# Optimization experiments

Measured on AMD Instinct MI355X. Metric: run time of the kernel, lower is better.

Reference implementation:

```python
import jax, jax.numpy as jnp
import numpy as np

N = 50000
E = 800000
IN = 3
H = 64
OUT = 128
L = 4


def _layernorm(x, w, b, eps=1e-5):
    mu = jnp.mean(x, axis=-1, keepdims=True)
    var = jnp.mean(jnp.square(x - mu), axis=-1, keepdims=True)
    return (x - mu) * jax.lax.rsqrt(var + eps) * w + b


def setup_inputs() -> dict:
    key = jax.random.key(0)
    ks = jax.random.split(key, 12)

    def lin(k, fan_in, shape):
        return jax.random.normal(k, shape, dtype=jnp.float32) / np.sqrt(fan_in)

    x = jax.random.normal(ks[0], (N, IN), dtype=jnp.float32)
    edge_index = jax.random.randint(ks[1], (2, E), 0, N, dtype=jnp.int32)
    return {
        "x": x,
        "edge_index": edge_index,
        "in_w": lin(ks[2], IN, (IN, H)), "in_b": jnp.zeros((H,), jnp.float32),
        "ew1": lin(ks[3], 2, (2, H)), "eb1": jnp.zeros((H,), jnp.float32),
        "ew2": lin(ks[4], H, (H, H)), "eb2": jnp.zeros((H,), jnp.float32),
        "cw1": lin(ks[5], H, (L, H, H)), "cb1": jnp.zeros((L, H), jnp.float32),
        "cw2": lin(ks[6], H, (L, H, H)), "cb2": jnp.zeros((L, H), jnp.float32),
        "lnw": jnp.ones((L, H), jnp.float32), "lnb": jnp.zeros((L, H), jnp.float32),
        "fw": lin(ks[7], H, (H, OUT)), "fb": jnp.zeros((OUT,), jnp.float32),
        "rw": lin(ks[8], H, (H, OUT)), "rb": jnp.zeros((OUT,), jnp.float32),
        "ow": jnp.ones((OUT,), jnp.float32), "ob": jnp.zeros((OUT,), jnp.float32),
    }


def reference(x, edge_index, in_w, in_b, ew1, eb1, ew2, eb2,
              cw1, cb1, cw2, cb2, lnw, lnb, fw, fb, rw, rb, ow, ob):
    pos = x[:, :2]
    row, col = edge_index[0], edge_index[1]  # source, target (PyG convention)
    rel_pos = pos[col] - pos[row]                              # [E, 2]
    edge_attr = jnp.maximum(rel_pos @ ew1 + eb1, 0.0) @ ew2 + eb2  # [E, H]

    h = x @ in_w + in_b  # [N, H]
    for i in range(L):
        identity = h
        # GINEConv (eps=0): mlp(x_i + sum_j relu(x_j + e_ij))
        msg = jax.nn.relu(h[row] + edge_attr)                  # [E, H]
        agg = jax.ops.segment_sum(msg, col, num_segments=N)    # [N, H]
        m = h + agg
        m = jnp.maximum(m @ cw1[i] + cb1[i], 0.0) @ cw2[i] + cb2[i]
        m = _layernorm(m, lnw[i], lnb[i])
        h = jax.nn.gelu(m, approximate=False) + identity

    out = (h @ fw + fb) + (h @ rw + rb)
    return _layernorm(out, ow, ob)
```

## Files before the change

### kernel.cpp

```cpp
#include <hip/hip_runtime.h>
#include <hip/hip_fp16.h>
#include <stdint.h>

#define NN 50000
#define NE 800000
#define SCAN_BLOCKS 196

typedef _Float16 half8v __attribute__((ext_vector_type(8)));
typedef float f32x4 __attribute__((ext_vector_type(4)));

static __device__ __forceinline__ __half2 u2h2(unsigned int u) {
    union { unsigned int u; __half2 h; } c; c.u = u; return c.h;
}
static __device__ __forceinline__ unsigned int h22u(__half2 h) {
    union { __half2 h; unsigned int u; } c; c.h = h; return c.u;
}

static __device__ __forceinline__ float4 fma4(float4 a, float s, float4 w) {
    a.x = fmaf(s, w.x, a.x); a.y = fmaf(s, w.y, a.y);
    a.z = fmaf(s, w.z, a.z); a.w = fmaf(s, w.w, a.w);
    return a;
}
static __device__ __forceinline__ void acc8(float* acc, float4 hv, float4 ev) {
    const unsigned int* hu = (const unsigned int*)&hv;
    const unsigned int* eu = (const unsigned int*)&ev;
    #pragma unroll
    for (int q = 0; q < 4; ++q) {
        float2 hf = __half22float2(u2h2(hu[q]));
        float2 ef = __half22float2(u2h2(eu[q]));
        acc[q * 2]     += fmaxf(hf.x + ef.x, 0.f);
        acc[q * 2 + 1] += fmaxf(hf.y + ef.y, 0.f);
    }
}

__global__ __launch_bounds__(256) void k_deg(const int* __restrict__ ei, int* __restrict__ offcur) {
    int e = blockIdx.x * 256 + threadIdx.x;
    atomicAdd(&offcur[ei[NE + e]], 1);
}

__global__ __launch_bounds__(256) void k_scanA(const int* __restrict__ off, int* __restrict__ part) {
    __shared__ int s[256];
    int t = threadIdx.x;
    int idx = blockIdx.x * 256 + t;
    int d = (idx < NN) ? off[idx] : 0;
    s[t] = d; __syncthreads();
    for (int o = 128; o > 0; o >>= 1) {
        if (t < o) s[t] += s[t + o];
        __syncthreads();
    }
    if (t == 0) part[blockIdx.x] = s[0];
}

__global__ __launch_bounds__(256) void k_scanB(int* __restrict__ part) {
    __shared__ int s[256];
    int t = threadIdx.x;
    int d = (t < SCAN_BLOCKS) ? part[t] : 0;
    s[t] = d; __syncthreads();
    #pragma unroll
    for (int o = 1; o < 256; o <<= 1) {
        int v = (t >= o) ? s[t - o] : 0;
        __syncthreads();
        s[t] += v;
        __syncthreads();
    }
    if (t < SCAN_BLOCKS) part[t] = s[t] - d;
}

__global__ __launch_bounds__(256) void k_scanC(int* __restrict__ off, const int* __restrict__ part) {
    __shared__ int s[256];
    int t = threadIdx.x;
    int idx = blockIdx.x * 256 + t;
    int d = (idx < NN) ? off[idx] : 0;
    s[t] = d; __syncthreads();
    #pragma unroll
    for (int o = 1; o < 256; o <<= 1) {
        int v = (t >= o) ? s[t - o] : 0;
        __syncthreads();
        s[t] += v;
        __syncthreads();
    }
    if (idx < NN) off[idx] = s[t] - d + part[blockIdx.x];
}

__global__ __launch_bounds__(256) void k_prep(const float* __restrict__ ew2, __half* __restrict__ w2f) {
    int tid = threadIdx.x;
    for (int i = tid; i < 4096; i += 256) {
        int k = i >> 6, n = i & 63;
        int kt = k >> 5, kin = k & 31;
        int quad = kin >> 3, j = kin & 7;
        int nt = n >> 4, nin = n & 15;
        w2f[(size_t)((kt * 4 + nt) * 64 + quad * 16 + nin) * 8 + j] = __float2half(ew2[i]);
    }
}

__global__ __launch_bounds__(256) void k_input(const float* __restrict__ x,
        const float* __restrict__ in_w, const float* __restrict__ in_b,
        __half* __restrict__ Ah) {
    int n = blockIdx.x * 4 + (threadIdx.x >> 6);
    int k = threadIdx.x & 63;
    const float* xr = x + (size_t)n * 3;
    float v = in_b[k] + xr[0] * in_w[k] + xr[1] * in_w[64 + k] + xr[2] * in_w[128 + k];
    Ah[(size_t)n * 64 + k] = __float2half(v);
}

__global__ __launch_bounds__(256) void k_edge(const float* __restrict__ x,
        const int* __restrict__ ei,
        const float* __restrict__ ew1, const float* __restrict__ eb1,
        const float* __restrict__ eb2, const __half* __restrict__ w2f,
        int* __restrict__ offcur, unsigned short* __restrict__ rows,
        __half* __restrict__ ea) {
    __shared__ float s_w1[128], s_b1[64], s_b2[64];
    __shared__ float s_rx[256], s_ry[256];
    __shared__ int s_pos[256];
    __shared__ __half s_d[4][16][80];
    int tid = threadIdx.x, lane = tid & 63, w = tid >> 6;

    half8v bf[8];
    {
        const half8v* W2F = (const half8v*)w2f;
        #pragma unroll
        for (int f = 0; f < 8; ++f) bf[f] = W2F[f * 64 + lane];
    }
    if (tid < 128) s_w1[tid] = ew1[tid];
    if (tid < 64) s_b1[tid] = eb1[tid];
    else if (tid < 128) s_b2[tid - 64] = eb2[tid - 64];
    int eb = blockIdx.x * 256;
    {
        int e = eb + tid;
        int r = ei[e], c = ei[NE + e];
        s_rx[tid] = x[(size_t)c * 3]     - x[(size_t)r * 3];
        s_ry[tid] = x[(size_t)c * 3 + 1] - x[(size_t)r * 3 + 1];
        int pos = atomicAdd(&offcur[c], 1);
        rows[pos] = (unsigned short)r;
        s_pos[tid] = pos;
    }
    __syncthreads();

    int lm = lane & 15, lq = lane >> 4;
    #pragma unroll
    for (int t = 0; t < 4; ++t) {
        int ebase = w * 64 + t * 16;
        float rx = s_rx[ebase + lm], ry = s_ry[ebase + lm];
        half8v a0, a1;
        #pragma unroll
        for (int j = 0; j < 8; ++j) {
            int k0 = lq * 8 + j;
            a0[j] = (_Float16)fmaxf(fmaf(rx, s_w1[k0], fmaf(ry, s_w1[64 + k0], s_b1[k0])), 0.f);
            int k1 = k0 + 32;
            a1[j] = (_Float16)fmaxf(fmaf(rx, s_w1[k1], fmaf(ry, s_w1[64 + k1], s_b1[k1])), 0.f);
        }
        f32x4 acc[4];
        #pragma unroll
        for (int nt = 0; nt < 4; ++nt) {
            float b = s_b2[nt * 16 + lm];
            acc[nt][0] = b; acc[nt][1] = b; acc[nt][2] = b; acc[nt][3] = b;
            acc[nt] = __builtin_amdgcn_mfma_f32_16x16x32_f16(a0, bf[nt],     acc[nt], 0, 0, 0);
            acc[nt] = __builtin_amdgcn_mfma_f32_16x16x32_f16(a1, bf[4 + nt], acc[nt], 0, 0, 0);
        }
        __builtin_amdgcn_wave_barrier();
        #pragma unroll
        for (int nt = 0; nt < 4; ++nt)
            #pragma unroll
            for (int r = 0; r < 4; ++r)
                s_d[w][lq * 4 + r][nt * 16 + lm] = __float2half(acc[nt][r]);
        __builtin_amdgcn_wave_barrier();
        int row = lane >> 2, seg = lane & 3;
        int pos = s_pos[w * 64 + t * 16 + row];
        uint4 v0 = *(const uint4*)&s_d[w][row][seg * 16];
        uint4 v1 = *(const uint4*)&s_d[w][row][seg * 16 + 8];
        uint4* dst = (uint4*)&ea[(size_t)pos * 64 + seg * 16];
        dst[0] = v0;
        dst[1] = v1;
        __builtin_amdgcn_wave_barrier();
    }
}

__global__ __launch_bounds__(256) void k_agg(const __half* __restrict__ Ah,
        const __half* __restrict__ ea, const unsigned short* __restrict__ rows,
        const int* __restrict__ offcur, __half* __restrict__ M) {
    const float4* A4 = (const float4*)Ah;
    const float4* E4 = (const float4*)ea;
    int w = threadIdx.x >> 6, lane = threadIdx.x & 63;
    int es = lane >> 3, oc = lane & 7;
    int n = blockIdx.x * 4 + w;
    int p0 = (n == 0) ? 0 : offcur[n - 1];
    int p1 = offcur[n];
    float acc[8] = {0,0,0,0,0,0,0,0};
    float accB[8] = {0,0,0,0,0,0,0,0};
    for (int base = p0; base < p1; base += 64) {
        int cnt = min(64, p1 - base);
        int rl = (int)rows[base + min(lane, cnt - 1)];
        int j = 0;
        for (; j + 16 <= cnt; j += 16) {
            int i0 = j + es, i1 = j + 8 + es;
            int r0 = __shfl(rl, i0, 64);
            int r1 = __shfl(rl, i1, 64);
            float4 h0 = A4[(size_t)r0 * 8 + oc];
            float4 h1 = A4[(size_t)r1 * 8 + oc];
            float4 e0 = E4[(size_t)(base + i0) * 8 + oc];
            float4 e1 = E4[(size_t)(base + i1) * 8 + oc];
            acc8(acc, h0, e0);
            acc8(accB, h1, e1);
        }
        for (; j < cnt; j += 8) {
            int i0 = j + es;
            bool valid = i0 < cnt;
            int ic = valid ? i0 : (cnt - 1);
            int r0 = __shfl(rl, ic, 64);
            float4 h0 = A4[(size_t)r0 * 8 + oc];
            float4 e0 = E4[(size_t)(base + ic) * 8 + oc];
            if (valid) acc8(acc, h0, e0);
        }
    }
    #pragma unroll
    for (int q = 0; q < 8; ++q) acc[q] += accB[q];
    #pragma unroll
    for (int m = 8; m < 64; m <<= 1) {
        #pragma unroll
        for (int q = 0; q < 8; ++q) acc[q] += __shfl_xor(acc[q], m, 64);
    }
    if (es == 0) {
        float4 sv = A4[(size_t)n * 8 + oc];
        const unsigned int* su = (const unsigned int*)&sv;
        unsigned int o[4];
        #pragma unroll
        for (int q = 0; q < 4; ++q) {
            float2 sf = __half22float2(u2h2(su[q]));
            o[q] = h22u(__floats2half2_rn(sf.x + acc[q * 2], sf.y + acc[q * 2 + 1]));
        }
        *(uint4*)&M[(size_t)n * 64 + oc * 8] = *(uint4*)&o[0];
    }
}

__global__ __launch_bounds__(256) void k_node(__half* __restrict__ Ah, const __half* __restrict__ M,
        const float* __restrict__ cw1, const float* __restrict__ cb1,
        const float* __restrict__ cw2, const float* __restrict__ cb2,
        const float* __restrict__ lnw, const float* __restrict__ lnb) {
    __shared__ float s_W1[64 * 64];
    __shared__ float s_W2[64 * 64];
    __shared__ float s_m[64 * 68];
    __shared__ float s_b1[64], s_b2[64], s_g[64], s_bt[64];
    int tid = threadIdx.x;
    for (int i = tid; i < 4096; i += 256) { s_W1[i] = cw1[i]; s_W2[i] = cw2[i]; }
    if (tid < 64) { s_b1[tid] = cb1[tid]; s_g[tid] = lnw[tid]; }
    else if (tid < 128) { s_b2[tid - 64] = cb2[tid - 64]; s_bt[tid - 64] = lnb[tid - 64]; }
    int nb = blockIdx.x * 64;
    {
        const uint4* M4 = (const uint4*)(M + (size_t)nb * 64);
        #pragma unroll
        for (int q = 0; q < 2; ++q) {
            int i = q * 256 + tid;
            int nl = i >> 3;
            int k8 = (i & 7) * 8;
            uint4 v = {0, 0, 0, 0};
            if (nb + nl < NN) v = M4[i];
            float* dst = &s_m[nl * 68 + k8];
            const unsigned int* vu = (const unsigned int*)&v;
            #pragma unroll
            for (int p = 0; p < 4; ++p) {
                float2 f = __half22float2(u2h2(vu[p]));
                dst[p * 2] = f.x; dst[p * 2 + 1] = f.y;
            }
        }
    }
    __syncthreads();

    int lane = tid & 63, w = tid >> 6;
    int cq = lane & 15, ng = lane >> 4;
    int rbase = w * 16 + ng * 4;
    int c0 = cq * 4;

    float4 acc[4];
    {
        float4 b1q = *(const float4*)&s_b1[c0];
        acc[0] = b1q; acc[1] = b1q; acc[2] = b1q; acc[3] = b1q;
    }
    #pragma unroll 4
    for (int k4 = 0; k4 < 16; ++k4) {
        float4 m0 = *(const float4*)&s_m[(rbase + 0) * 68 + k4 * 4];
        float4 m1 = *(const float4*)&s_m[(rbase + 1) * 68 + k4 * 4];
        float4 m2 = *(const float4*)&s_m[(rbase + 2) * 68 + k4 * 4];
        float4 m3 = *(const float4*)&s_m[(rbase + 3) * 68 + k4 * 4];
        #pragma unroll
        for (int kk = 0; kk < 4; ++kk) {
            float4 w4 = *(const float4*)&s_W1[(k4 * 4 + kk) * 64 + c0];
            acc[0] = fma4(acc[0], ((const float*)&m0)[kk], w4);
            acc[1] = fma4(acc[1], ((const float*)&m1)[kk], w4);
            acc[2] = fma4(acc[2], ((const float*)&m2)[kk], w4);
            acc[3] = fma4(acc[3], ((const float*)&m3)[kk], w4);
        }
    }
    __builtin_amdgcn_wave_barrier();
    #pragma unroll
    for (int j = 0; j < 4; ++j) {
        float4 u;
        u.x = fmaxf(acc[j].x, 0.f); u.y = fmaxf(acc[j].y, 0.f);
        u.z = fmaxf(acc[j].z, 0.f); u.w = fmaxf(acc[j].w, 0.f);
        *(float4*)&s_m[(rbase + j) * 68 + c0] = u;
    }
    __builtin_amdgcn_wave_barrier();

    {
        float4 b2q = *(const float4*)&s_b2[c0];
        acc[0] = b2q; acc[1] = b2q; acc[2] = b2q; acc[3] = b2q;
    }
    #pragma unroll 4
    for (int k4 = 0; k4 < 16; ++k4) {
        float4 m0 = *(const float4*)&s_m[(rbase + 0) * 68 + k4 * 4];
        float4 m1 = *(const float4*)&s_m[(rbase + 1) * 68 + k4 * 4];
        float4 m2 = *(const float4*)&s_m[(rbase + 2) * 68 + k4 * 4];
        float4 m3 = *(const float4*)&s_m[(rbase + 3) * 68 + k4 * 4];
        #pragma unroll
        for (int kk = 0; kk < 4; ++kk) {
            float4 w4 = *(const float4*)&s_W2[(k4 * 4 + kk) * 64 + c0];
            acc[0] = fma4(acc[0], ((const float*)&m0)[kk], w4);
            acc[1] = fma4(acc[1], ((const float*)&m1)[kk], w4);
            acc[2] = fma4(acc[2], ((const float*)&m2)[kk], w4);
            acc[3] = fma4(acc[3], ((const float*)&m3)[kk], w4);
        }
    }

    float4 gq  = *(const float4*)&s_g[c0];
    float4 btq = *(const float4*)&s_bt[c0];
    #pragma unroll
    for (int j = 0; j < 4; ++j) {
        float4 v = acc[j];
        float sum = v.x + v.y + v.z + v.w;
        float sq  = v.x * v.x + v.y * v.y + v.z * v.z + v.w * v.w;
        #pragma unroll
        for (int m = 1; m < 16; m <<= 1) {
            sum += __shfl_xor(sum, m, 64);
            sq  += __shfl_xor(sq, m, 64);
        }
        float mu  = sum * (1.f / 64.f);
        float var = sq * (1.f / 64.f) - mu * mu;
        float rs  = rsqrtf(var + 1e-5f);
        int n = nb + rbase + j;
        if (n < NN) {
            uint2 iu = *(const uint2*)&Ah[(size_t)n * 64 + c0];
            float2 i0 = __half22float2(u2h2(iu.x));
            float2 i1 = __half22float2(u2h2(iu.y));
            float4 o;
            float y;
            y = (v.x - mu) * rs * gq.x + btq.x; o.x = 0.5f * y * (1.f + erff(y * 0.70710678118654752f)) + i0.x;
            y = (v.y - mu) * rs * gq.y + btq.y; o.y = 0.5f * y * (1.f + erff(y * 0.70710678118654752f)) + i0.y;
            y = (v.z - mu) * rs * gq.z + btq.z; o.z = 0.5f * y * (1.f + erff(y * 0.70710678118654752f)) + i1.x;
            y = (v.w - mu) * rs * gq.w + btq.w; o.w = 0.5f * y * (1.f + erff(y * 0.70710678118654752f)) + i1.y;
            uint2 ou;
            ou.x = h22u(__floats2half2_rn(o.x, o.y));
            ou.y = h22u(__floats2half2_rn(o.z, o.w));
            *(uint2*)&Ah[(size_t)n * 64 + c0] = ou;
        }
    }
}

__global__ __launch_bounds__(256) void k_final(const __half* __restrict__ Ah,
        const float* __restrict__ fw, const float* __restrict__ fb,
        const float* __restrict__ rw, const float* __restrict__ rb,
        const float* __restrict__ ow, const float* __restrict__ ob,
        float* __restrict__ out) {
    __shared__ float s_W[64 * 128];
    __shared__ float s_h[32 * 68];
    __shared__ float s_b[128];
    __shared__ float s_red[32][4];
    int tid = threadIdx.x;
    for (int i = tid; i < 8192; i += 256) s_W[i] = fw[i] + rw[i];
    if (tid < 128) s_b[tid] = fb[tid] + rb[tid];
    int nb = blockIdx.x * 32;
    for (int i = tid; i < 2048; i += 256) {
        int nl = i >> 6, k = i & 63;
        int n = nb + nl;
        s_h[nl * 68 + k] = (n < NN) ? __half2float(Ah[(size_t)n * 64 + k]) : 0.f;
    }
    __syncthreads();

    int lane = tid & 63, w = tid >> 6;
    int chh = w & 1, nh = w >> 1;
    int cq = lane & 15, ng = lane >> 4;
    int c0 = chh * 64 + cq * 4;
    int rbase = nh * 16 + ng * 4;

    float4 acc[4];
    {
        float4 bq = *(const float4*)&s_b[c0];
        acc[0] = bq; acc[1] = bq; acc[2] = bq; acc[3] = bq;
    }
    #pragma unroll 4
    for (int k4 = 0; k4 < 16; ++k4) {
        float4 m0 = *(const float4*)&s_h[(rbase + 0) * 68 + k4 * 4];
        float4 m1 = *(const float4*)&s_h[(rbase + 1) * 68 + k4 * 4];
        float4 m2 = *(const float4*)&s_h[(rbase + 2) * 68 + k4 * 4];
        float4 m3 = *(const float4*)&s_h[(rbase + 3) * 68 + k4 * 4];
        #pragma unroll
        for (int kk = 0; kk < 4; ++kk) {
            float4 w4 = *(const float4*)&s_W[(k4 * 4 + kk) * 128 + c0];
            acc[0] = fma4(acc[0], ((const float*)&m0)[kk], w4);
            acc[1] = fma4(acc[1], ((const float*)&m1)[kk], w4);
            acc[2] = fma4(acc[2], ((const float*)&m2)[kk], w4);
            acc[3] = fma4(acc[3], ((const float*)&m3)[kk], w4);
        }
    }
    #pragma unroll
    for (int j = 0; j < 4; ++j) {
        float4 v = acc[j];
        float sum = v.x + v.y + v.z + v.w;
        float sq  = v.x * v.x + v.y * v.y + v.z * v.z + v.w * v.w;
        #pragma unroll
        for (int m = 1; m < 16; m <<= 1) {
            sum += __shfl_xor(sum, m, 64);
            sq  += __shfl_xor(sq, m, 64);
        }
        if (cq == 0) {
            s_red[rbase + j][chh * 2]     = sum;
            s_red[rbase + j][chh * 2 + 1] = sq;
        }
    }
    __syncthreads();
    float4 gq = *(const float4*)&ow[c0];
    float4 bq = *(const float4*)&ob[c0];
    #pragma unroll
    for (int j = 0; j < 4; ++j) {
        int nl = rbase + j;
        int n = nb + nl;
        float tsum = s_red[nl][0] + s_red[nl][2];
        float tsq  = s_red[nl][1] + s_red[nl][3];
        float mu  = tsum * (1.f / 128.f);
        float var = tsq * (1.f / 128.f) - mu * mu;
        float rs  = rsqrtf(var + 1e-5f);
        if (n < NN) {
            float4 v = acc[j];
            float4 o;
            o.x = (v.x - mu) * rs * gq.x + bq.x;
            o.y = (v.y - mu) * rs * gq.y + bq.y;
            o.z = (v.z - mu) * rs * gq.z + bq.z;
            o.w = (v.w - mu) * rs * gq.w + bq.w;
            *(float4*)&out[(size_t)n * 128 + c0] = o;
        }
    }
}

extern "C" void kernel_launch(void* const* d_in, const int* in_sizes, int n_in,
                              void* d_out, int out_size, void* d_ws, size_t ws_size,
                              hipStream_t stream) {
    const float* x    = (const float*)d_in[0];
    const int*   ei   = (const int*)d_in[1];
    const float* in_w = (const float*)d_in[2];
    const float* in_b = (const float*)d_in[3];
    const float* ew1  = (const float*)d_in[4];
    const float* eb1  = (const float*)d_in[5];
    const float* ew2  = (const float*)d_in[6];
    const float* eb2  = (const float*)d_in[7];
    const float* cw1  = (const float*)d_in[8];
    const float* cb1  = (const float*)d_in[9];
    const float* cw2  = (const float*)d_in[10];
    const float* cb2  = (const float*)d_in[11];
    const float* lnw  = (const float*)d_in[12];
    const float* lnb  = (const float*)d_in[13];
    const float* fw   = (const float*)d_in[14];
    const float* fb   = (const float*)d_in[15];
    const float* rw   = (const float*)d_in[16];
    const float* rb   = (const float*)d_in[17];
    const float* ow   = (const float*)d_in[18];
    const float* ob   = (const float*)d_in[19];
    float* out = (float*)d_out;

    char* ws = (char*)d_ws;
    __half*         ea   = (__half*)ws;
    __half*         Ah   = (__half*)(ws + 102400000);
    unsigned short* rows = (unsigned short*)(ws + 108800000);
    int*            off  = (int*)(ws + 110400000);
    __half*         M    = (__half*)(ws + 110600016);
    int*            part = (int*)M;
    __half*         w2f  = (__half*)((char*)M + 100000);

    (void)hipMemsetAsync(off, 0, (NN + 1) * sizeof(int), stream);
    k_deg<<<NE / 256, 256, 0, stream>>>(ei, off);
    k_scanA<<<SCAN_BLOCKS, 256, 0, stream>>>(off, part);
    k_scanB<<<1, 256, 0, stream>>>(part);
    k_scanC<<<SCAN_BLOCKS, 256, 0, stream>>>(off, part);
    k_prep<<<1, 256, 0, stream>>>(ew2, w2f);
    k_input<<<NN / 4, 256, 0, stream>>>(x, in_w, in_b, Ah);
    k_edge<<<NE / 256, 256, 0, stream>>>(x, ei, ew1, eb1, eb2, w2f, off, rows, ea);

    const int nodeBlocks = (NN + 63) / 64;
    for (int l = 0; l < 4; ++l) {
        k_agg<<<NN / 4, 256, 0, stream>>>(Ah, ea, rows, off, M);
        k_node<<<nodeBlocks, 256, 0, stream>>>(Ah, M,
            cw1 + (size_t)l * 4096, cb1 + (size_t)l * 64,
            cw2 + (size_t)l * 4096, cb2 + (size_t)l * 64,
            lnw + (size_t)l * 64,   lnb + (size_t)l * 64);
    }
    k_final<<<(NN + 31) / 32, 256, 0, stream>>>(Ah, fw, fb, rw, rb, ow, ob, out);
}
```

Measured before the change: 477.4 us.

## Fuse edge aggregation into node MLP kernel with ping-pong feature buffers

Merges the per-layer aggregation kernel into the node MLP/LayerNorm kernel. Each block gathers neighbour messages for its 64 nodes directly into shared memory in fp32, which removes the intermediate fp16 M buffer round trip and one launch per layer. Two feature buffers are now ping-ponged so no block overwrites features that other blocks still read. The rows store in the edge kernel is also moved after the MFMA work. The trade-off is fewer blocks (782 instead of 12500) and less parallelism for the irregular gather. The weight staging also now shares a block with the latency-bound gather.

Result: slower. 614.9 us (+28.8%).

```diff
diff --git a/kernel.cpp b/kernel.cpp
--- a/kernel.cpp
+++ b/kernel.cpp
@@ -125,13 +125,14 @@
     if (tid < 64) s_b1[tid] = eb1[tid];
     else if (tid < 128) s_b2[tid - 64] = eb2[tid - 64];
     int eb = blockIdx.x * 256;
+    int my_r, my_pos;
     {
         int e = eb + tid;
         int r = ei[e], c = ei[NE + e];
         s_rx[tid] = x[(size_t)c * 3]     - x[(size_t)r * 3];
         s_ry[tid] = x[(size_t)c * 3 + 1] - x[(size_t)r * 3 + 1];
         int pos = atomicAdd(&offcur[c], 1);
-        rows[pos] = (unsigned short)r;
+        my_r = r; my_pos = pos;
         s_pos[tid] = pos;
     }
     __syncthreads();
@@ -173,66 +174,13 @@
         dst[1] = v1;
         __builtin_amdgcn_wave_barrier();
     }
-}
-
-__global__ __launch_bounds__(256) void k_agg(const __half* __restrict__ Ah,
+    rows[my_pos] = (unsigned short)my_r;
+}
+
+__global__ __launch_bounds__(256) void k_layer(const __half* __restrict__ Ain,
+        __half* __restrict__ Aout,
         const __half* __restrict__ ea, const unsigned short* __restrict__ rows,
-        const int* __restrict__ offcur, __half* __restrict__ M) {
-    const float4* A4 = (const float4*)Ah;
-    const float4* E4 = (const float4*)ea;
-    int w = threadIdx.x >> 6, lane = threadIdx.x & 63;
-    int es = lane >> 3, oc = lane & 7;
-    int n = blockIdx.x * 4 + w;
-    int p0 = (n == 0) ? 0 : offcur[n - 1];
-    int p1 = offcur[n];
-    float acc[8] = {0,0,0,0,0,0,0,0};
-    float accB[8] = {0,0,0,0,0,0,0,0};
-    for (int base = p0; base < p1; base += 64) {
-        int cnt = min(64, p1 - base);
-        int rl = (int)rows[base + min(lane, cnt - 1)];
-        int j = 0;
-        for (; j + 16 <= cnt; j += 16) {
-            int i0 = j + es, i1 = j + 8 + es;
-            int r0 = __shfl(rl, i0, 64);
-            int r1 = __shfl(rl, i1, 64);
-            float4 h0 = A4[(size_t)r0 * 8 + oc];
-            float4 h1 = A4[(size_t)r1 * 8 + oc];
-            float4 e0 = E4[(size_t)(base + i0) * 8 + oc];
-            float4 e1 = E4[(size_t)(base + i1) * 8 + oc];
-            acc8(acc, h0, e0);
-            acc8(accB, h1, e1);
-        }
-        for (; j < cnt; j += 8) {
-            int i0 = j + es;
-            bool valid = i0 < cnt;
-            int ic = valid ? i0 : (cnt - 1);
-            int r0 = __shfl(rl, ic, 64);
-            float4 h0 = A4[(size_t)r0 * 8 + oc];
-            float4 e0 = E4[(size_t)(base + ic) * 8 + oc];
-            if (valid) acc8(acc, h0, e0);
-        }
-    }
-    #pragma unroll
-    for (int q = 0; q < 8; ++q) acc[q] += accB[q];
-    #pragma unroll
-    for (int m = 8; m < 64; m <<= 1) {
-        #pragma unroll
-        for (int q = 0; q < 8; ++q) acc[q] += __shfl_xor(acc[q], m, 64);
-    }
-    if (es == 0) {
-        float4 sv = A4[(size_t)n * 8 + oc];
-        const unsigned int* su = (const unsigned int*)&sv;
-        unsigned int o[4];
-        #pragma unroll
-        for (int q = 0; q < 4; ++q) {
-            float2 sf = __half22float2(u2h2(su[q]));
-            o[q] = h22u(__floats2half2_rn(sf.x + acc[q * 2], sf.y + acc[q * 2 + 1]));
-        }
-        *(uint4*)&M[(size_t)n * 64 + oc * 8] = *(uint4*)&o[0];
-    }
-}
-
-__global__ __launch_bounds__(256) void k_node(__half* __restrict__ Ah, const __half* __restrict__ M,
+        const int* __restrict__ off,
         const float* __restrict__ cw1, const float* __restrict__ cb1,
         const float* __restrict__ cw2, const float* __restrict__ cb2,
         const float* __restrict__ lnw, const float* __restrict__ lnb) {
@@ -244,28 +192,72 @@
     for (int i = tid; i < 4096; i += 256) { s_W1[i] = cw1[i]; s_W2[i] = cw2[i]; }
     if (tid < 64) { s_b1[tid] = cb1[tid]; s_g[tid] = lnw[tid]; }
     else if (tid < 128) { s_b2[tid - 64] = cb2[tid - 64]; s_bt[tid - 64] = lnb[tid - 64]; }
+
     int nb = blockIdx.x * 64;
-    {
-        const uint4* M4 = (const uint4*)(M + (size_t)nb * 64);
-        #pragma unroll
-        for (int q = 0; q < 2; ++q) {
-            int i = q * 256 + tid;
-            int nl = i >> 3;
-            int k8 = (i & 7) * 8;
-            uint4 v = {0, 0, 0, 0};
-            if (nb + nl < NN) v = M4[i];
-            float* dst = &s_m[nl * 68 + k8];
-            const unsigned int* vu = (const unsigned int*)&v;
+    int lane = tid & 63, w = tid >> 6;
+
+    {
+        const float4* A4 = (const float4*)Ain;
+        const float4* E4 = (const float4*)ea;
+        int es = lane >> 3, oc = lane & 7;
+        for (int t = 0; t < 16; ++t) {
+            int nl = w * 16 + t;
+            int n = nb + nl;
+            float acc[8] = {0,0,0,0,0,0,0,0};
+            float accB[8] = {0,0,0,0,0,0,0,0};
+            int p0 = 0, p1 = 0;
+            if (n < NN) { p0 = (n == 0) ? 0 : off[n - 1]; p1 = off[n]; }
+            for (int base = p0; base < p1; base += 64) {
+                int cnt = min(64, p1 - base);
+                int rl = (int)rows[base + min(lane, cnt - 1)];
+                int j = 0;
+                for (; j + 16 <= cnt; j += 16) {
+                    int i0 = j + es, i1 = j + 8 + es;
+                    int r0 = __shfl(rl, i0, 64);
+                    int r1 = __shfl(rl, i1, 64);
+                    float4 h0 = A4[(size_t)r0 * 8 + oc];
+                    float4 h1 = A4[(size_t)r1 * 8 + oc];
+                    float4 e0 = E4[(size_t)(base + i0) * 8 + oc];
+                    float4 e1 = E4[(size_t)(base + i1) * 8 + oc];
+                    acc8(acc, h0, e0);
+                    acc8(accB, h1, e1);
+                }
+                for (; j < cnt; j += 8) {
+                    int i0 = j + es;
+                    bool valid = i0 < cnt;
+                    int ic = valid ? i0 : (cnt - 1);
+                    int r0 = __shfl(rl, ic, 64);
+                    float4 h0 = A4[(size_t)r0 * 8 + oc];
+                    float4 e0 = E4[(size_t)(base + ic) * 8 + oc];
+                    if (valid) acc8(acc, h0, e0);
+                }
+            }
             #pragma unroll
-            for (int p = 0; p < 4; ++p) {
-                float2 f = __half22float2(u2h2(vu[p]));
-                dst[p * 2] = f.x; dst[p * 2 + 1] = f.y;
+            for (int q = 0; q < 8; ++q) acc[q] += accB[q];
+            #pragma unroll
+            for (int m = 8; m < 64; m <<= 1) {
+                #pragma unroll
+                for (int q = 0; q < 8; ++q) acc[q] += __shfl_xor(acc[q], m, 64);
             }
+            if (es == 0) {
+                if (n < NN) {
+                    float4 sv = A4[(size_t)n * 8 + oc];
+                    const unsigned int* su = (const unsigned int*)&sv;
+                    #pragma unroll
+                    for (int q = 0; q < 4; ++q) {
+                        float2 sf = __half22float2(u2h2(su[q]));
+                        acc[q * 2]     += sf.x;
+                        acc[q * 2 + 1] += sf.y;
+                    }
+                }
+                float* dst = &s_m[nl * 68 + oc * 8];
+                *(float4*)dst       = *(float4*)&acc[0];
+                *(float4*)(dst + 4) = *(float4*)&acc[4];
+            }
         }
     }
     __syncthreads();
 
-    int lane = tid & 63, w = tid >> 6;
     int cq = lane & 15, ng = lane >> 4;
     int rbase = w * 16 + ng * 4;
     int c0 = cq * 4;
@@ -337,7 +329,7 @@
         float rs  = rsqrtf(var + 1e-5f);
         int n = nb + rbase + j;
         if (n < NN) {
-            uint2 iu = *(const uint2*)&Ah[(size_t)n * 64 + c0];
+            uint2 iu = *(const uint2*)&Ain[(size_t)n * 64 + c0];
             float2 i0 = __half22float2(u2h2(iu.x));
             float2 i1 = __half22float2(u2h2(iu.y));
             float4 o;
@@ -349,7 +341,7 @@
             uint2 ou;
             ou.x = h22u(__floats2half2_rn(o.x, o.y));
             ou.y = h22u(__floats2half2_rn(o.z, o.w));
-            *(uint2*)&Ah[(size_t)n * 64 + c0] = ou;
+            *(uint2*)&Aout[(size_t)n * 64 + c0] = ou;
         }
     }
 }
@@ -466,12 +458,12 @@
 
     char* ws = (char*)d_ws;
     __half*         ea   = (__half*)ws;
-    __half*         Ah   = (__half*)(ws + 102400000);
-    unsigned short* rows = (unsigned short*)(ws + 108800000);
-    int*            off  = (int*)(ws + 110400000);
-    __half*         M    = (__half*)(ws + 110600016);
-    int*            part = (int*)M;
-    __half*         w2f  = (__half*)((char*)M + 100000);
+    __half*         Ah0  = (__half*)(ws + 102400000);
+    __half*         Ah1  = (__half*)(ws + 108800000);
+    unsigned short* rows = (unsigned short*)(ws + 115200000);
+    int*            off  = (int*)(ws + 116800000);
+    int*            part = (int*)(ws + 117000016);
+    __half*         w2f  = (__half*)(ws + 117100016);
 
     (void)hipMemsetAsync(off, 0, (NN + 1) * sizeof(int), stream);
     k_deg<<<NE / 256, 256, 0, stream>>>(ei, off);
@@ -479,16 +471,18 @@
     k_scanB<<<1, 256, 0, stream>>>(part);
     k_scanC<<<SCAN_BLOCKS, 256, 0, stream>>>(off, part);
     k_prep<<<1, 256, 0, stream>>>(ew2, w2f);
-    k_input<<<NN / 4, 256, 0, stream>>>(x, in_w, in_b, Ah);
+    k_input<<<NN / 4, 256, 0, stream>>>(x, in_w, in_b, Ah0);
     k_edge<<<NE / 256, 256, 0, stream>>>(x, ei, ew1, eb1, eb2, w2f, off, rows, ea);
 
     const int nodeBlocks = (NN + 63) / 64;
+    __half* Ain = Ah0;
+    __half* Aout = Ah1;
     for (int l = 0; l < 4; ++l) {
-        k_agg<<<NN / 4, 256, 0, stream>>>(Ah, ea, rows, off, M);
-        k_node<<<nodeBlocks, 256, 0, stream>>>(Ah, M,
+        k_layer<<<nodeBlocks, 256, 0, stream>>>(Ain, Aout, ea, rows, off,
             cw1 + (size_t)l * 4096, cb1 + (size_t)l * 64,
             cw2 + (size_t)l * 4096, cb2 + (size_t)l * 64,
             lnw + (size_t)l * 64,   lnb + (size_t)l * 64);
-    }
-    k_final<<<(NN + 31) / 32, 256, 0, stream>>>(Ah, fw, fb, rw, rb, ow, ob, out);
-}
+        __half* tmp = Ain; Ain = Aout; Aout = tmp;
+    }
+    k_final<<<(NN + 31) / 32, 256, 0, stream>>>(Ain, fw, fb, rw, rb, ow, ob, out);
+}
```

## Use fp16 MFMA for node MLP with prepacked conv weights

Applied to the files above, without the earlier changes.

The node-update kernel now runs both 64x64 matmuls on MFMA 16x16x32 f16 instructions instead of fp32 FMA loops. It reads weights that k_prep (now 9 blocks) converts once into fp16 fragment layout, and LayerNorm statistics are reduced from the MFMA accumulator layout. This removes the per-block fp32 weight staging into LDS (32KB) and the scalar FMA work, at the cost of fp16 rounding of the hidden activation. Separately, the rows[] scatter store in k_edge is moved to the end of the kernel.

After: 406.4 us. 14.9% less time.

```diff
diff --git a/kernel.cpp b/kernel.cpp
--- a/kernel.cpp
+++ b/kernel.cpp
@@ -82,14 +82,24 @@
     if (idx < NN) off[idx] = s[t] - d + part[blockIdx.x];
 }
 
-__global__ __launch_bounds__(256) void k_prep(const float* __restrict__ ew2, __half* __restrict__ w2f) {
+__global__ __launch_bounds__(256) void k_prep(const float* __restrict__ ew2,
+        const float* __restrict__ cw1, const float* __restrict__ cw2,
+        __half* __restrict__ wf) {
+    int b = blockIdx.x;
+    const float* src;
+    if (b == 0) src = ew2;
+    else {
+        int l = (b - 1) >> 1;
+        src = ((b - 1) & 1) ? (cw2 + (size_t)l * 4096) : (cw1 + (size_t)l * 4096);
+    }
+    __half* dst = wf + (size_t)b * 4096;
     int tid = threadIdx.x;
     for (int i = tid; i < 4096; i += 256) {
         int k = i >> 6, n = i & 63;
         int kt = k >> 5, kin = k & 31;
         int quad = kin >> 3, j = kin & 7;
         int nt = n >> 4, nin = n & 15;
-        w2f[(size_t)((kt * 4 + nt) * 64 + quad * 16 + nin) * 8 + j] = __float2half(ew2[i]);
+        dst[(size_t)((kt * 4 + nt) * 64 + quad * 16 + nin) * 8 + j] = __float2half(src[i]);
     }
 }
 
@@ -125,13 +135,14 @@
     if (tid < 64) s_b1[tid] = eb1[tid];
     else if (tid < 128) s_b2[tid - 64] = eb2[tid - 64];
     int eb = blockIdx.x * 256;
+    int my_r, my_pos;
     {
         int e = eb + tid;
         int r = ei[e], c = ei[NE + e];
         s_rx[tid] = x[(size_t)c * 3]     - x[(size_t)r * 3];
         s_ry[tid] = x[(size_t)c * 3 + 1] - x[(size_t)r * 3 + 1];
         int pos = atomicAdd(&offcur[c], 1);
-        rows[pos] = (unsigned short)r;
+        my_r = r; my_pos = pos;
         s_pos[tid] = pos;
     }
     __syncthreads();
@@ -173,6 +184,7 @@
         dst[1] = v1;
         __builtin_amdgcn_wave_barrier();
     }
+    rows[my_pos] = (unsigned short)my_r;
 }
 
 __global__ __launch_bounds__(256) void k_agg(const __half* __restrict__ Ah,
@@ -233,123 +245,109 @@
 }
 
 __global__ __launch_bounds__(256) void k_node(__half* __restrict__ Ah, const __half* __restrict__ M,
-        const float* __restrict__ cw1, const float* __restrict__ cb1,
-        const float* __restrict__ cw2, const float* __restrict__ cb2,
+        const __half* __restrict__ w1f, const __half* __restrict__ w2f,
+        const float* __restrict__ cb1, const float* __restrict__ cb2,
         const float* __restrict__ lnw, const float* __restrict__ lnb) {
-    __shared__ float s_W1[64 * 64];
-    __shared__ float s_W2[64 * 64];
-    __shared__ float s_m[64 * 68];
+    __shared__ __half s_u[4][16][72];
     __shared__ float s_b1[64], s_b2[64], s_g[64], s_bt[64];
-    int tid = threadIdx.x;
-    for (int i = tid; i < 4096; i += 256) { s_W1[i] = cw1[i]; s_W2[i] = cw2[i]; }
+    int tid = threadIdx.x, lane = tid & 63, w = tid >> 6;
+    int lm = lane & 15, lq = lane >> 4;
+
+    half8v bw1[8], bw2[8];
+    {
+        const half8v* W1F = (const half8v*)w1f;
+        const half8v* W2F = (const half8v*)w2f;
+        #pragma unroll
+        for (int f = 0; f < 8; ++f) { bw1[f] = W1F[f * 64 + lane]; bw2[f] = W2F[f * 64 + lane]; }
+    }
     if (tid < 64) { s_b1[tid] = cb1[tid]; s_g[tid] = lnw[tid]; }
     else if (tid < 128) { s_b2[tid - 64] = cb2[tid - 64]; s_bt[tid - 64] = lnb[tid - 64]; }
+    __syncthreads();
+
     int nb = blockIdx.x * 64;
-    {
-        const uint4* M4 = (const uint4*)(M + (size_t)nb * 64);
-        #pragma unroll
-        for (int q = 0; q < 2; ++q) {
-            int i = q * 256 + tid;
-            int nl = i >> 3;
-            int k8 = (i & 7) * 8;
-            uint4 v = {0, 0, 0, 0};
-            if (nb + nl < NN) v = M4[i];
-            float* dst = &s_m[nl * 68 + k8];
-            const unsigned int* vu = (const unsigned int*)&v;
+    int na = nb + w * 16 + lm;
+    int nac = min(na, NN - 1);
+
+    const uint4* M4 = (const uint4*)M;
+    uint4 a0u = M4[(size_t)nac * 8 + lq];
+    uint4 a1u = M4[(size_t)nac * 8 + 4 + lq];
+    half8v a0 = *(const half8v*)&a0u;
+    half8v a1 = *(const half8v*)&a1u;
+
+    f32x4 acc[4];
+    #pragma unroll
+    for (int nt = 0; nt < 4; ++nt) {
+        float b = s_b1[nt * 16 + lm];
+        acc[nt][0] = b; acc[nt][1] = b; acc[nt][2] = b; acc[nt][3] = b;
+        acc[nt] = __builtin_amdgcn_mfma_f32_16x16x32_f16(a0, bw1[nt],     acc[nt], 0, 0, 0);
+        acc[nt] = __builtin_amdgcn_mfma_f32_16x16x32_f16(a1, bw1[4 + nt], acc[nt], 0, 0, 0);
+    }
+    __builtin_amdgcn_wave_barrier();
+    #pragma unroll
+    for (int nt = 0; nt < 4; ++nt)
+        #pragma unroll
+        for (int r = 0; r < 4; ++r)
+            s_u[w][lq * 4 + r][nt * 16 + lm] = __float2half(fmaxf(acc[nt][r], 0.f));
+    __builtin_amdgcn_wave_barrier();
+
+    half8v u0 = *(const half8v*)&s_u[w][lm][lq * 8];
+    half8v u1 = *(const half8v*)&s_u[w][lm][32 + lq * 8];
+    #pragma unroll
+    for (int nt = 0; nt < 4; ++nt) {
+        float b = s_b2[nt * 16 + lm];
+        acc[nt][0] = b; acc[nt][1] = b; acc[nt][2] = b; acc[nt][3] = b;
+        acc[nt] = __builtin_amdgcn_mfma_f32_16x16x32_f16(u0, bw2[nt],     acc[nt], 0, 0, 0);
+        acc[nt] = __builtin_amdgcn_mfma_f32_16x16x32_f16(u1, bw2[4 + nt], acc[nt], 0, 0, 0);
+    }
+
+    float S[4], SQ[4];
+    #pragma unroll
+    for (int r = 0; r < 4; ++r) {
+        S[r]  = acc[0][r] + acc[1][r] + acc[2][r] + acc[3][r];
+        SQ[r] = acc[0][r] * acc[0][r] + acc[1][r] * acc[1][r]
+              + acc[2][r] * acc[2][r] + acc[3][r] * acc[3][r];
+    }
+    #pragma unroll
+    for (int m = 1; m < 16; m <<= 1) {
+        #pragma unroll
+        for (int r = 0; r < 4; ++r) {
+            S[r]  += __shfl_xor(S[r], m, 64);
+            SQ[r] += __shfl_xor(SQ[r], m, 64);
+        }
+    }
+    __builtin_amdgcn_wave_barrier();
+    #pragma unroll
+    for (int r = 0; r < 4; ++r) {
+        float mu  = S[r] * (1.f / 64.f);
+        float var = SQ[r] * (1.f / 64.f) - mu * mu;
+        float rs  = rsqrtf(var + 1e-5f);
+        #pragma unroll
+        for (int nt = 0; nt < 4; ++nt) {
+            int c = nt * 16 + lm;
+            float y = (acc[nt][r] - mu) * rs * s_g[c] + s_bt[c];
+            float ge = 0.5f * y * (1.f + erff(y * 0.70710678118654752f));
+            s_u[w][lq * 4 + r][c] = __float2half(ge);
+        }
+    }
+    __builtin_amdgcn_wave_barrier();
+
+    #pragma unroll
+    for (int it = 0; it < 2; ++it) {
+        int ck = lq + 4 * it;
+        int n = nb + w * 16 + lm;
+        if (n < NN) {
+            uint4 ge8 = *(const uint4*)&s_u[w][lm][ck * 8];
+            uint4 id8 = *(const uint4*)&Ah[(size_t)n * 64 + ck * 8];
+            const unsigned int* gu = (const unsigned int*)&ge8;
+            const unsigned int* iu = (const unsigned int*)&id8;
+            unsigned int o[4];
             #pragma unroll
             for (int p = 0; p < 4; ++p) {
-                float2 f = __half22float2(u2h2(vu[p]));
-                dst[p * 2] = f.x; dst[p * 2 + 1] = f.y;
+                float2 gf = __half22float2(u2h2(gu[p]));
+                float2 iff = __half22float2(u2h2(iu[p]));
+                o[p] = h22u(__floats2half2_rn(gf.x + iff.x, gf.y + iff.y));
             }
-        }
-    }
-    __syncthreads();
-
-    int lane = tid & 63, w = tid >> 6;
-    int cq = lane & 15, ng = lane >> 4;
-    int rbase = w * 16 + ng * 4;
-    int c0 = cq * 4;
-
-    float4 acc[4];
-    {
-        float4 b1q = *(const float4*)&s_b1[c0];
-        acc[0] = b1q; acc[1] = b1q; acc[2] = b1q; acc[3] = b1q;
-    }
-    #pragma unroll 4
-    for (int k4 = 0; k4 < 16; ++k4) {
-        float4 m0 = *(const float4*)&s_m[(rbase + 0) * 68 + k4 * 4];
-        float4 m1 = *(const float4*)&s_m[(rbase + 1) * 68 + k4 * 4];
-        float4 m2 = *(const float4*)&s_m[(rbase + 2) * 68 + k4 * 4];
-        float4 m3 = *(const float4*)&s_m[(rbase + 3) * 68 + k4 * 4];
-        #pragma unroll
-        for (int kk = 0; kk < 4; ++kk) {
-            float4 w4 = *(const float4*)&s_W1[(k4 * 4 + kk) * 64 + c0];
-            acc[0] = fma4(acc[0], ((const float*)&m0)[kk], w4);
-            acc[1] = fma4(acc[1], ((const float*)&m1)[kk], w4);
-            acc[2] = fma4(acc[2], ((const float*)&m2)[kk], w4);
-            acc[3] = fma4(acc[3], ((const float*)&m3)[kk], w4);
-        }
-    }
-    __builtin_amdgcn_wave_barrier();
-    #pragma unroll
-    for (int j = 0; j < 4; ++j) {
-        float4 u;
-        u.x = fmaxf(acc[j].x, 0.f); u.y = fmaxf(acc[j].y, 0.f);
-        u.z = fmaxf(acc[j].z, 0.f); u.w = fmaxf(acc[j].w, 0.f);
-        *(float4*)&s_m[(rbase + j) * 68 + c0] = u;
-    }
-    __builtin_amdgcn_wave_barrier();
-
-    {
-        float4 b2q = *(const float4*)&s_b2[c0];
-        acc[0] = b2q; acc[1] = b2q; acc[2] = b2q; acc[3] = b2q;
-    }
-    #pragma unroll 4
-    for (int k4 = 0; k4 < 16; ++k4) {
-        float4 m0 = *(const float4*)&s_m[(rbase + 0) * 68 + k4 * 4];
-        float4 m1 = *(const float4*)&s_m[(rbase + 1) * 68 + k4 * 4];
-        float4 m2 = *(const float4*)&s_m[(rbase + 2) * 68 + k4 * 4];
-        float4 m3 = *(const float4*)&s_m[(rbase + 3) * 68 + k4 * 4];
-        #pragma unroll
-        for (int kk = 0; kk < 4; ++kk) {
-            float4 w4 = *(const float4*)&s_W2[(k4 * 4 + kk) * 64 + c0];
-            acc[0] = fma4(acc[0], ((const float*)&m0)[kk], w4);
-            acc[1] = fma4(acc[1], ((const float*)&m1)[kk], w4);
-            acc[2] = fma4(acc[2], ((const float*)&m2)[kk], w4);
-            acc[3] = fma4(acc[3], ((const float*)&m3)[kk], w4);
-        }
-    }
-
-    float4 gq  = *(const float4*)&s_g[c0];
-    float4 btq = *(const float4*)&s_bt[c0];
-    #pragma unroll
-    for (int j = 0; j < 4; ++j) {
-        float4 v = acc[j];
-        float sum = v.x + v.y + v.z + v.w;
-        float sq  = v.x * v.x + v.y * v.y + v.z * v.z + v.w * v.w;
-        #pragma unroll
-        for (int m = 1; m < 16; m <<= 1) {
-            sum += __shfl_xor(sum, m, 64);
-            sq  += __shfl_xor(sq, m, 64);
-        }
-        float mu  = sum * (1.f / 64.f);
-        float var = sq * (1.f / 64.f) - mu * mu;
-        float rs  = rsqrtf(var + 1e-5f);
-        int n = nb + rbase + j;
-        if (n < NN) {
-            uint2 iu = *(const uint2*)&Ah[(size_t)n * 64 + c0];
-            float2 i0 = __half22float2(u2h2(iu.x));
-            float2 i1 = __half22float2(u2h2(iu.y));
-            float4 o;
-            float y;
-            y = (v.x - mu) * rs * gq.x + btq.x; o.x = 0.5f * y * (1.f + erff(y * 0.70710678118654752f)) + i0.x;
-            y = (v.y - mu) * rs * gq.y + btq.y; o.y = 0.5f * y * (1.f + erff(y * 0.70710678118654752f)) + i0.y;
-            y = (v.z - mu) * rs * gq.z + btq.z; o.z = 0.5f * y * (1.f + erff(y * 0.70710678118654752f)) + i1.x;
-            y = (v.w - mu) * rs * gq.w + btq.w; o.w = 0.5f * y * (1.f + erff(y * 0.70710678118654752f)) + i1.y;
-            uint2 ou;
-            ou.x = h22u(__floats2half2_rn(o.x, o.y));
-            ou.y = h22u(__floats2half2_rn(o.z, o.w));
-            *(uint2*)&Ah[(size_t)n * 64 + c0] = ou;
+            *(uint4*)&Ah[(size_t)n * 64 + ck * 8] = *(uint4*)&o[0];
         }
     }
 }
@@ -470,25 +468,25 @@
     unsigned short* rows = (unsigned short*)(ws + 108800000);
     int*            off  = (int*)(ws + 110400000);
     __half*         M    = (__half*)(ws + 110600016);
+    __half*         wf   = (__half*)(ws + 117000016);
     int*            part = (int*)M;
-    __half*         w2f  = (__half*)((char*)M + 100000);
 
     (void)hipMemsetAsync(off, 0, (NN + 1) * sizeof(int), stream);
     k_deg<<<NE / 256, 256, 0, stream>>>(ei, off);
     k_scanA<<<SCAN_BLOCKS, 256, 0, stream>>>(off, part);
     k_scanB<<<1, 256, 0, stream>>>(part);
     k_scanC<<<SCAN_BLOCKS, 256, 0, stream>>>(off, part);
-    k_prep<<<1, 256, 0, stream>>>(ew2, w2f);
+    k_prep<<<9, 256, 0, stream>>>(ew2, cw1, cw2, wf);
     k_input<<<NN / 4, 256, 0, stream>>>(x, in_w, in_b, Ah);
-    k_edge<<<NE / 256, 256, 0, stream>>>(x, ei, ew1, eb1, eb2, w2f, off, rows, ea);
+    k_edge<<<NE / 256, 256, 0, stream>>>(x, ei, ew1, eb1, eb2, wf, off, rows, ea);
 
     const int nodeBlocks = (NN + 63) / 64;
     for (int l = 0; l < 4; ++l) {
         k_agg<<<NN / 4, 256, 0, stream>>>(Ah, ea, rows, off, M);
         k_node<<<nodeBlocks, 256, 0, stream>>>(Ah, M,
-            cw1 + (size_t)l * 4096, cb1 + (size_t)l * 64,
-            cw2 + (size_t)l * 4096, cb2 + (size_t)l * 64,
-            lnw + (size_t)l * 64,   lnb + (size_t)l * 64);
+            wf + (size_t)(1 + 2 * l) * 4096, wf + (size_t)(2 + 2 * l) * 4096,
+            cb1 + (size_t)l * 64, cb2 + (size_t)l * 64,
+            lnw + (size_t)l * 64, lnb + (size_t)l * 64);
     }
     k_final<<<(NN + 31) / 32, 256, 0, stream>>>(Ah, fw, fb, rw, rb, ow, ob, out);
 }
```
